# Kernel optimization log

Measured on AMD Instinct MI355X. Metric: run time of the kernel, lower is better.

Reference implementation:

```python
import jax, jax.numpy as jnp
import numpy as np
import math

N, D = 4096, 1024

def setup_inputs() -> dict:
    key = jax.random.key(0)
    ks = jax.random.split(key, 12)
    x = jax.random.normal(ks[0], (N, D), dtype=jnp.float32)
    attention_mask = jax.random.randint(ks[1], (N, N), 0, 2).astype(jnp.float32)
    learnable_mask = jax.random.randint(ks[2], (N, N), 0, 2).astype(jnp.float32)
    boundary_mask = jax.random.randint(ks[3], (N, 1), 0, 2).astype(jnp.float32)
    s = 1.0 / math.sqrt(D)
    W_q = jax.random.normal(ks[4], (D, D), dtype=jnp.float32) * s
    b_q = jax.random.normal(ks[5], (D,), dtype=jnp.float32) * s
    W_k = jax.random.normal(ks[6], (D, D), dtype=jnp.float32) * s
    b_k = jax.random.normal(ks[7], (D,), dtype=jnp.float32) * s
    W_v = jax.random.normal(ks[8], (D, D), dtype=jnp.float32) * s
    b_v = jax.random.normal(ks[9], (D,), dtype=jnp.float32) * s
    connection = jax.random.normal(ks[10], (D, D), dtype=jnp.float32) * s
    bias = jnp.ones((1,), dtype=jnp.float32) * 0.01
    return {"x": x, "attention_mask": attention_mask, "learnable_mask": learnable_mask,
            "boundary_mask": boundary_mask, "W_q": W_q, "b_q": b_q, "W_k": W_k, "b_k": b_k,
            "W_v": W_v, "b_v": b_v, "connection": connection, "bias": bias}

def reference(x, attention_mask, learnable_mask, boundary_mask,
              W_q, b_q, W_k, b_k, W_v, b_v, connection, bias):
    # Linear layers (torch Linear: x @ W.T + b)
    q = x @ W_q.T + b_q            # [N, D]
    k = x @ W_k.T + b_k            # [N, D]
    v = x @ W_v.T + b_v            # [N, D]
    d_head = k.shape[-1]
    attention_logits = (q @ k.T) / jnp.sqrt(jnp.asarray(d_head, x.dtype))  # [N, N]
    connection_logits = (q @ connection) @ k.T + bias                      # [N, N]
    # straight-through hard sigmoid mask
    soft_mask = jax.nn.sigmoid(connection_logits)
    st_mask = (soft_mask > 0.5).astype(x.dtype) - jax.lax.stop_gradient(soft_mask) + soft_mask
    lm = st_mask * learnable_mask
    mask = attention_mask + lm
    mask = -10000.0 * (1.0 - mask)
    attention = jax.nn.softmax(attention_logits + mask, axis=-1)  # [N, N]
    x_residual = attention @ v                                    # [N, D]
    out = boundary_mask * x_residual + (1.0 - boundary_mask) * x
    return out
```

## Files before the change

kernel.cpp:

```cpp
#include <hip/hip_runtime.h>
#include <cstdint>


typedef __attribute__((ext_vector_type(8))) short short8;
typedef __attribute__((ext_vector_type(4))) float f32x4;
typedef __attribute__((ext_vector_type(4))) float f4v;
typedef __attribute__((ext_vector_type(4))) unsigned short u16x4;
typedef __attribute__((ext_vector_type(8))) unsigned short u16x8;

typedef unsigned short u16;
typedef unsigned char u8;

__device__ __forceinline__ u16 f2bf(float f) {
  unsigned u = __float_as_uint(f);
  u += 0x7fffu + ((u >> 16) & 1u);
  return (u16)(u >> 16);
}
__device__ __forceinline__ float bf2f(u16 h) {
  return __uint_as_float(((unsigned)h) << 16);
}

__device__ __forceinline__ void gld16(void* lds, const void* g) {
  __builtin_amdgcn_global_load_lds(
      (__attribute__((address_space(1))) void*)g,
      (__attribute__((address_space(3))) void*)lds,
      16, 0, 0);
}


__global__ void prep_bm(const float* __restrict__ bm, int* __restrict__ idx,
                        int* __restrict__ cntp) {
  __shared__ int ps[1024];
  const int t = threadIdx.x;
  int loc[4];
  int c = 0;
#pragma unroll
  for (int e = 0; e < 4; e++) {
    int r = t * 4 + e;
    if (bm[r] != 0.0f) loc[c++] = r;
  }
  ps[t] = c;
  __syncthreads();
  for (int off = 1; off < 1024; off <<= 1) {
    int v = (t >= off) ? ps[t - off] : 0;
    __syncthreads();
    ps[t] += v;
    __syncthreads();
  }
  int base = ps[t] - c;
  for (int i = 0; i < c; i++) idx[base + i] = loc[i];
  int cnt = ps[1023];
  if (t == 0) cntp[0] = cnt;
  for (int r = cnt + t; r < 4096; r += 1024) idx[r] = 0;
}

__global__ void prep_x(const float* __restrict__ x, u16* __restrict__ xs3) {
  int id = blockIdx.x * 256 + threadIdx.x;
  int flat = id * 4;
  int n = flat >> 10, i = flat & 1023;
  f4v v = *(const f4v*)(x + (size_t)flat);
  u16x4 hi, lo;
#pragma unroll
  for (int e = 0; e < 4; e++) {
    float f = v[e];
    u16 h = f2bf(f);
    hi[e] = h;
    lo[e] = f2bf(f - bf2f(h));
  }
  size_t base = (size_t)n * 3072 + i;
  *(u16x4*)(xs3 + base) = hi;
  *(u16x4*)(xs3 + base + 1024) = lo;
  *(u16x4*)(xs3 + base + 2048) = hi;
}

__global__ void prep_w(const float* __restrict__ Wq, const float* __restrict__ Wk,
                       const float* __restrict__ Wv, u16* __restrict__ W3) {
  int id = blockIdx.x * 256 + threadIdx.x;
  int flat = id * 4;
  int o = flat >> 10, i = flat & 1023;
  const float* src = (o < 1024) ? (Wq + (size_t)o * 1024)
                   : (o < 2048) ? (Wk + (size_t)(o - 1024) * 1024)
                                : (Wv + (size_t)(o - 2048) * 1024);
  f4v v = *(const f4v*)(src + i);
  u16x4 hi, lo;
#pragma unroll
  for (int e = 0; e < 4; e++) {
    u16 h = f2bf(v[e]);
    hi[e] = h;
    lo[e] = f2bf(v[e] - bf2f(h));
  }
  size_t base = (size_t)o * 3072 + i;
  *(u16x4*)(W3 + base) = hi;
  *(u16x4*)(W3 + base + 1024) = hi;
  *(u16x4*)(W3 + base + 2048) = lo;
}

__global__ void prep_bias(const float* __restrict__ bq, const float* __restrict__ bk,
                          const float* __restrict__ bv, float* __restrict__ bp) {
  int id = blockIdx.x * 256 + threadIdx.x;
  float v = (id < 1024) ? bq[id] : (id < 2048) ? bk[id - 1024] : bv[id - 2048];
  bp[id] = v;
}

__global__ void prep_c(const float* __restrict__ C, u16* __restrict__ C3) {
  __shared__ float t[32][33];
  int lx = threadIdx.x & 31, ly = threadIdx.x >> 5;
  int i0 = blockIdx.x * 32, j0 = blockIdx.y * 32;
#pragma unroll
  for (int r = 0; r < 32; r += 8)
    t[ly + r][lx] = C[(size_t)(i0 + ly + r) * 1024 + j0 + lx];
  __syncthreads();
#pragma unroll
  for (int r = 0; r < 32; r += 8) {
    float f = t[lx][ly + r];
    u16 h = f2bf(f);
    u16 l = f2bf(f - bf2f(h));
    size_t o = (size_t)(j0 + ly + r) * 3072 + i0 + lx;
    C3[o] = h;
    C3[o + 1024] = h;
    C3[o + 2048] = l;
  }
}


struct EpiG1 {
  const float* bp; u16* qs3; u16* k3; u16* vt; int mode;
  __device__ void operator()(int r, int c, float v) const {
    if (mode == 0) {
      v += bp[1024 + c];
      u16 h = f2bf(v);
      u16 l = f2bf(v - bf2f(h));
      size_t b = (size_t)r * 3072 + c;
      k3[b] = h; k3[b + 1024] = h; k3[b + 2048] = l;
    } else if (mode == 1) {
      v += bp[c];
      u16 h = f2bf(v);
      u16 l = f2bf(v - bf2f(h));
      size_t b = (size_t)r * 3072 + c;
      qs3[b] = h; qs3[b + 1024] = l; qs3[b + 2048] = h;
    } else {
      v += bp[2048 + r];
      vt[(size_t)r * 4096 + c] = f2bf(v);
    }
  }
};

struct EpiQCS {
  u16* qc3; u16* Sc; int isS;
  __device__ void operator()(int r, int c, float v) const {
    if (isS) {
      Sc[(size_t)r * 4096 + c] = f2bf(v);
    } else {
      u16 h = f2bf(v);
      u16 l = f2bf(v - bf2f(h));
      size_t b = (size_t)r * 3072 + c;
      qc3[b] = h; qc3[b + 1024] = l; qc3[b + 2048] = h;
    }
  }
};

struct EpiCL {
  u8* st; float b0;
  __device__ void operator()(int r, int c, float v) const {
    st[(size_t)r * 4096 + c] = (v + b0 > 0.f) ? 1 : 0;
  }
};

struct EpiPart {
  float* part; const int* idx; int cnt;
  __device__ void operator()(int r, int c, float v) const {
    if (r < cnt) part[(size_t)idx[r] * 1024 + c] = v;
  }
};

template <class Epi>
__device__ __forceinline__ void gemm_core(
    const u16* __restrict__ A, const u16* __restrict__ B,
    int lda, int ldb, int K, int mBase, int nBase,
    const int* __restrict__ ridx, Epi epi) {
  __shared__ __align__(16) u16 lA[128 * 64];
  __shared__ __align__(16) u16 lB[128 * 64];
  const int tid = threadIdx.x;
  const int wave = tid >> 6, lane = tid & 63;
  const int wm = wave & 1, wn = wave >> 1;
  const int lane16 = lane & 15, quad = lane >> 4;

  const int srow = tid >> 3;
  const int gchunk = ((tid & 7) ^ (srow & 7)) * 8;
  const u16* aPi[4];
#pragma unroll
  for (int i = 0; i < 4; i++) {
    int row = mBase + srow + 32 * i;
    int g = ridx ? ridx[row] : row;
    aPi[i] = A + (size_t)g * lda + gchunk;
  }
  const u16* bP = B + (size_t)(nBase + srow) * ldb + gchunk;
  const int woff = wave * 1024;

  const int rsw = lane16 & 7;
  const u16* raB = lA + (wm * 64 + lane16) * 64;
  const u16* rbB = lB + (wn * 64 + lane16) * 64;

  f32x4 acc[4][4];
#pragma unroll
  for (int i = 0; i < 4; i++)
#pragma unroll
    for (int j = 0; j < 4; j++) acc[i][j] = (f32x4){0.f, 0.f, 0.f, 0.f};

  for (int k0 = 0; k0 < K; k0 += 64) {
#pragma unroll
    for (int i = 0; i < 4; i++) {
      gld16((char*)lA + i * 4096 + woff, aPi[i] + k0);
      gld16((char*)lB + i * 4096 + woff, bP + (size_t)(32 * i) * ldb + k0);
    }
    __syncthreads();
    short8 af[2][4], bfr[2][4];
#pragma unroll
    for (int s = 0; s < 2; s++) {
      const int sl = (((s << 2) + quad) ^ rsw) * 8;
#pragma unroll
      for (int j = 0; j < 4; j++) {
        af[s][j]  = *(const short8*)(raB + j * 1024 + sl);
        bfr[s][j] = *(const short8*)(rbB + j * 1024 + sl);
      }
    }
#pragma unroll
    for (int s = 0; s < 2; s++)
#pragma unroll
      for (int im = 0; im < 4; im++)
#pragma unroll
        for (int in = 0; in < 4; in++)
          acc[im][in] = __builtin_amdgcn_mfma_f32_16x16x32_bf16(
              af[s][im], bfr[s][in], acc[im][in], 0, 0, 0);
    __syncthreads();
  }

#pragma unroll
  for (int im = 0; im < 4; im++)
#pragma unroll
    for (int in = 0; in < 4; in++)
#pragma unroll
      for (int i = 0; i < 4; i++) {
        int r = mBase + wm * 64 + im * 16 + quad * 4 + i;
        int c = nBase + wn * 64 + in * 16 + lane16;
        epi(r, c, acc[im][in][i]);
      }
}

__global__ __launch_bounds__(256, 2) void gemm_g1(
    const u16* __restrict__ xs3, const u16* __restrict__ W3,
    const float* __restrict__ bp, u16* __restrict__ qs3,
    u16* __restrict__ k3, u16* __restrict__ vt,
    const int* __restrict__ idx, const int* __restrict__ cntp) {
  const int bid = blockIdx.x;
  const u16 *A, *B;
  const int* rx = nullptr;
  int K, mB, nB, mode;
  if (bid < 256) {
    A = xs3; B = W3 + (size_t)1024 * 3072; K = 3072;
    mB = (bid >> 3) * 128; nB = (bid & 7) * 128; mode = 0;
  } else if (bid < 512) {
    const int t = bid - 256;
    mB = (t >> 3) * 128;
    if (mB >= cntp[0]) return;
    A = xs3; B = W3; K = 3072; nB = (t & 7) * 128; rx = idx; mode = 1;
  } else {
    const int t = bid - 512;
    A = W3 + (size_t)2048 * 3072; B = xs3; K = 1024;
    mB = (t & 7) * 128; nB = (t >> 3) * 128; mode = 2;
  }
  gemm_core(A, B, 3072, 3072, K, mB, nB, rx, EpiG1{bp, qs3, k3, vt, mode});
}

__global__ __launch_bounds__(256, 2) void gemm_qc_s(
    const u16* __restrict__ qs3, const u16* __restrict__ C3,
    const u16* __restrict__ k3, u16* __restrict__ qc3, u16* __restrict__ Sc,
    const int* __restrict__ cntp) {
  const int bid = blockIdx.x;
  const int cnt = cntp[0];
  const u16* B;
  int K, mB, nB, isS;
  if (bid < 256) {
    mB = (bid >> 3) * 128;
    if (mB >= cnt) return;
    B = C3; K = 3072; nB = (bid & 7) * 128; isS = 0;
  } else {
    const int t = bid - 256;
    mB = (t >> 5) * 128;
    if (mB >= cnt) return;
    B = k3; K = 1024; nB = (t & 31) * 128; isS = 1;
  }
  gemm_core(qs3, B, 3072, 3072, K, mB, nB, nullptr, EpiQCS{qc3, Sc, isS});
}

__global__ __launch_bounds__(256, 2) void gemm_cl(
    const u16* __restrict__ qc3, const u16* __restrict__ k3,
    const float* __restrict__ bias, u8* __restrict__ st,
    const int* __restrict__ cntp) {
  const int bid = blockIdx.x;
  const int mBase = (bid >> 5) * 128;
  if (mBase >= cntp[0]) return;
  gemm_core(qc3, k3, 3072, 3072, 3072, mBase, (bid & 31) * 128, nullptr,
            EpiCL{st, bias[0]});
}

__global__ __launch_bounds__(256, 2) void gemm_pv(
    const u16* __restrict__ P, const u16* __restrict__ vt,
    float* __restrict__ p01, float* __restrict__ p23,
    const int* __restrict__ idx, const int* __restrict__ cntp) {
  const int bid = blockIdx.x;
  const int z = bid >> 8, rem = bid & 255;
  const int cnt = cntp[0];
  const int mBase = (rem >> 3) * 128;
  if (mBase >= cnt) return;
  float* base = ((z < 2) ? p01 : p23) + (size_t)(z & 1) * (4096ull * 1024ull);
  const size_t kOff = (size_t)z * 1024;
  gemm_core(P + kOff, vt + kOff, 4096, 4096, 1024, mBase, (rem & 7) * 128,
            nullptr, EpiPart{base, idx, cnt});
}

__global__ void reduce_out(const float* __restrict__ x, const float* __restrict__ bm,
                           const float* __restrict__ p01, const float* __restrict__ p23,
                           float* __restrict__ out) {
  int id = blockIdx.x * 256 + threadIdx.x;
  int flat = id * 4;
  int r = flat >> 10;
  float b = bm[r];
  f4v xv = *(const f4v*)(x + (size_t)flat);
  f4v o;
  if (b != 0.0f) {
    const size_t SL = (size_t)4096 * 1024;
    f4v a0 = *(const f4v*)(p01 + (size_t)flat);
    f4v a1 = *(const f4v*)(p01 + SL + flat);
    f4v a2 = *(const f4v*)(p23 + (size_t)flat);
    f4v a3 = *(const f4v*)(p23 + SL + flat);
#pragma unroll
    for (int e = 0; e < 4; e++)
      o[e] = b * ((a0[e] + a1[e]) + (a2[e] + a3[e])) + (1.0f - b) * xv[e];
  } else {
    o = xv;
  }
  *(f4v*)(out + (size_t)flat) = o;
}

__global__ __launch_bounds__(256) void mask_softmax(
    const u16* __restrict__ Sc, const u8* __restrict__ st,
    const float* __restrict__ am, const float* __restrict__ lm,
    u16* __restrict__ P, const int* __restrict__ idx,
    const int* __restrict__ cntp) {
  const int n = blockIdx.x, tid = threadIdx.x;
  if (n >= cntp[0]) return;
  const int orow = idx[n];
  const int lane = tid & 63, wave = tid >> 6;
  const u16* Srow = Sc + (size_t)n * 4096;
  const u8* Trow = st + (size_t)n * 4096;
  const float* Arow = am + (size_t)orow * 4096;
  const float* Lrow = lm + (size_t)orow * 4096;

  float lg[16];
  float mx = -3.4e38f;
#pragma unroll
  for (int j = 0; j < 2; j++) {
    int base = (tid + 256 * j) * 8;
    u16x8 s8 = *(const u16x8*)(Srow + base);
    unsigned long long t8 = *(const unsigned long long*)(Trow + base);
    f4v a0 = *(const f4v*)(Arow + base), a1 = *(const f4v*)(Arow + base + 4);
    f4v l0 = *(const f4v*)(Lrow + base), l1 = *(const f4v*)(Lrow + base + 4);
#pragma unroll
    for (int e = 0; e < 8; e++) {
      float stv = ((t8 >> (8 * e)) & 1ull) ? 1.f : 0.f;
      float a = (e < 4) ? a0[e] : a1[e - 4];
      float l = (e < 4) ? l0[e] : l1[e - 4];
      float mv = a + stv * l;
      float v = bf2f(s8[e]) * 0.03125f - 10000.f * (1.f - mv);
      lg[j * 8 + e] = v;
      mx = fmaxf(mx, v);
    }
  }
#pragma unroll
  for (int o = 32; o; o >>= 1) mx = fmaxf(mx, __shfl_xor(mx, o));
  __shared__ float smax[4], ssum[4];
  if (lane == 0) smax[wave] = mx;
  __syncthreads();
  mx = fmaxf(fmaxf(smax[0], smax[1]), fmaxf(smax[2], smax[3]));

  float sum = 0.f;
#pragma unroll
  for (int i = 0; i < 16; i++) { lg[i] = __expf(lg[i] - mx); sum += lg[i]; }
#pragma unroll
  for (int o = 32; o; o >>= 1) sum += __shfl_xor(sum, o);
  if (lane == 0) ssum[wave] = sum;
  __syncthreads();
  float inv = 1.f / (ssum[0] + ssum[1] + ssum[2] + ssum[3]);

  u16* Pr = P + (size_t)n * 4096;
#pragma unroll
  for (int j = 0; j < 2; j++) {
    int base = (tid + 256 * j) * 8;
    u16x8 o8;
#pragma unroll
    for (int e = 0; e < 8; e++) o8[e] = f2bf(lg[j * 8 + e] * inv);
    *(u16x8*)(Pr + base) = o8;
  }
}


extern "C" void kernel_launch(void* const* d_in, const int* in_sizes, int n_in,
                              void* d_out, int out_size, void* d_ws, size_t ws_size,
                              hipStream_t stream) {
  const float* x    = (const float*)d_in[0];
  const float* am   = (const float*)d_in[1];
  const float* lm   = (const float*)d_in[2];
  const float* bm   = (const float*)d_in[3];
  const float* Wq   = (const float*)d_in[4];
  const float* bq   = (const float*)d_in[5];
  const float* Wk   = (const float*)d_in[6];
  const float* bk   = (const float*)d_in[7];
  const float* Wv   = (const float*)d_in[8];
  const float* bv   = (const float*)d_in[9];
  const float* Cc   = (const float*)d_in[10];
  const float* bias = (const float*)d_in[11];
  float* out = (float*)d_out;
  char* ws = (char*)d_ws;

  if (ws_size < 0xB010000) return;

  u16*  xs3 = (u16*) (ws + 0x0000000);
  u16*  W3  = (u16*) (ws + 0x1800000);
  u16*  C3  = (u16*) (ws + 0x2A00000);
  float* bp = (float*)(ws + 0x3000000);
  int*  idx = (int*)  (ws + 0x3004000);
  int*  cnt = (int*)  (ws + 0x3008000);
  u16*  qs3 = (u16*) (ws + 0x3010000);
  u16*  qc3 = (u16*) (ws + 0x4810000);
  u16*  k3  = (u16*) (ws + 0x6010000);
  u16*  vt  = (u16*) (ws + 0x7810000);
  u16*  Sc  = (u16*) (ws + 0x8010000);
  u8*   st  = (u8*)  (ws + 0xA010000);
  u16*  P   = (u16*) (ws + 0x0000000);
  float* parts01 = (float*)(ws + 0x4810000);
  float* parts23 = (float*)(ws + 0x8010000);

  prep_bm  <<<1, 1024, 0, stream>>>(bm, idx, cnt);
  prep_x   <<<4096, 256, 0, stream>>>(x, xs3);
  prep_w   <<<3072, 256, 0, stream>>>(Wq, Wk, Wv, W3);
  prep_bias<<<12,   256, 0, stream>>>(bq, bk, bv, bp);
  prep_c   <<<dim3(32, 32), 256, 0, stream>>>(Cc, C3);

  gemm_g1<<<768, 256, 0, stream>>>(xs3, W3, bp, qs3, k3, vt, idx, cnt);
  gemm_qc_s<<<1280, 256, 0, stream>>>(qs3, C3, k3, qc3, Sc, cnt);
  gemm_cl<<<1024, 256, 0, stream>>>(qc3, k3, bias, st, cnt);
  mask_softmax<<<4096, 256, 0, stream>>>(Sc, st, am, lm, P, idx, cnt);
  gemm_pv<<<1024, 256, 0, stream>>>(P, vt, parts01, parts23, idx, cnt);
  reduce_out<<<4096, 256, 0, stream>>>(x, bm, parts01, parts23, out);
}
```

Measured before the change: 417.9 us.

## Precompute Wq-connection product to fuse q and qc projections into one GEMM

```diff
diff --git a/kernel.cpp b/kernel.cpp
--- a/kernel.cpp
+++ b/kernel.cpp
@@ -27,104 +27,141 @@
       16, 0, 0);
 }
 
-
-__global__ void prep_bm(const float* __restrict__ bm, int* __restrict__ idx,
-                        int* __restrict__ cntp) {
-  __shared__ int ps[1024];
-  const int t = threadIdx.x;
-  int loc[4];
-  int c = 0;
-#pragma unroll
-  for (int e = 0; e < 4; e++) {
-    int r = t * 4 + e;
-    if (bm[r] != 0.0f) loc[c++] = r;
-  }
-  ps[t] = c;
-  __syncthreads();
-  for (int off = 1; off < 1024; off <<= 1) {
-    int v = (t >= off) ? ps[t - off] : 0;
+__global__ __launch_bounds__(256) void prep_all(
+    const float* __restrict__ x, const float* __restrict__ Wq,
+    const float* __restrict__ Wk, const float* __restrict__ Wv,
+    const float* __restrict__ bq, const float* __restrict__ bk,
+    const float* __restrict__ bv, const float* __restrict__ C,
+    const float* __restrict__ bm,
+    u16* __restrict__ xs3, u16* __restrict__ W3, u16* __restrict__ Wqm,
+    u16* __restrict__ WqT3, u16* __restrict__ C3,
+    float* __restrict__ bp, float* __restrict__ b1,
+    int* __restrict__ idx, int* __restrict__ cntp) {
+  __shared__ float tb[32][33];
+  __shared__ int ps[256];
+  const int bid = blockIdx.x, t = threadIdx.x;
+
+  if (bid < 4096) {
+    int flat = (bid * 256 + t) * 4;
+    int n = flat >> 10, i = flat & 1023;
+    f4v v = *(const f4v*)(x + (size_t)flat);
+    u16x4 hi, lo;
+#pragma unroll
+    for (int e = 0; e < 4; e++) {
+      u16 h = f2bf(v[e]);
+      hi[e] = h;
+      lo[e] = f2bf(v[e] - bf2f(h));
+    }
+    size_t base = (size_t)n * 3072 + i;
+    *(u16x4*)(xs3 + base) = hi;
+    *(u16x4*)(xs3 + base + 1024) = lo;
+    *(u16x4*)(xs3 + base + 2048) = hi;
+  } else if (bid < 6144) {
+    int flat = ((bid - 4096) * 256 + t) * 4;
+    int o = flat >> 10, i = flat & 1023;
+    const float* src = (o < 1024) ? (Wk + (size_t)o * 1024)
+                                  : (Wv + (size_t)(o - 1024) * 1024);
+    f4v v = *(const f4v*)(src + i);
+    u16x4 hi, lo;
+#pragma unroll
+    for (int e = 0; e < 4; e++) {
+      u16 h = f2bf(v[e]);
+      hi[e] = h;
+      lo[e] = f2bf(v[e] - bf2f(h));
+    }
+    size_t base = (size_t)o * 3072 + i;
+    *(u16x4*)(W3 + base) = hi;
+    *(u16x4*)(W3 + base + 1024) = hi;
+    *(u16x4*)(W3 + base + 2048) = lo;
+  } else if (bid < 7168) {
+    int flat = ((bid - 6144) * 256 + t) * 4;
+    int o = flat >> 10, i = flat & 1023;
+    f4v v = *(const f4v*)(Wq + (size_t)o * 1024 + i);
+    u16x4 hi, lo;
+#pragma unroll
+    for (int e = 0; e < 4; e++) {
+      u16 h = f2bf(v[e]);
+      hi[e] = h;
+      lo[e] = f2bf(v[e] - bf2f(h));
+    }
+    size_t base = (size_t)o * 3072 + i;
+    *(u16x4*)(Wqm + base) = hi;
+    *(u16x4*)(Wqm + base + 1024) = hi;
+    *(u16x4*)(Wqm + base + 2048) = lo;
+  } else if (bid < 8192) {
+    int tt = bid - 7168;
+    int lx = t & 31, ly = t >> 5;
+    int i0 = (tt & 31) * 32, j0 = (tt >> 5) * 32;
+#pragma unroll
+    for (int r = 0; r < 32; r += 8)
+      tb[ly + r][lx] = Wq[(size_t)(i0 + ly + r) * 1024 + j0 + lx];
     __syncthreads();
-    ps[t] += v;
+#pragma unroll
+    for (int r = 0; r < 32; r += 8) {
+      float f = tb[lx][ly + r];
+      u16 h = f2bf(f);
+      u16 l = f2bf(f - bf2f(h));
+      size_t o = (size_t)(j0 + ly + r) * 3072 + i0 + lx;
+      WqT3[o] = h;
+      WqT3[o + 1024] = h;
+      WqT3[o + 2048] = l;
+    }
+  } else if (bid < 9216) {
+    int tt = bid - 8192;
+    int lx = t & 31, ly = t >> 5;
+    int i0 = (tt & 31) * 32, j0 = (tt >> 5) * 32;
+#pragma unroll
+    for (int r = 0; r < 32; r += 8)
+      tb[ly + r][lx] = C[(size_t)(i0 + ly + r) * 1024 + j0 + lx];
     __syncthreads();
-  }
-  int base = ps[t] - c;
-  for (int i = 0; i < c; i++) idx[base + i] = loc[i];
-  int cnt = ps[1023];
-  if (t == 0) cntp[0] = cnt;
-  for (int r = cnt + t; r < 4096; r += 1024) idx[r] = 0;
-}
-
-__global__ void prep_x(const float* __restrict__ x, u16* __restrict__ xs3) {
-  int id = blockIdx.x * 256 + threadIdx.x;
-  int flat = id * 4;
-  int n = flat >> 10, i = flat & 1023;
-  f4v v = *(const f4v*)(x + (size_t)flat);
-  u16x4 hi, lo;
-#pragma unroll
-  for (int e = 0; e < 4; e++) {
-    float f = v[e];
-    u16 h = f2bf(f);
-    hi[e] = h;
-    lo[e] = f2bf(f - bf2f(h));
-  }
-  size_t base = (size_t)n * 3072 + i;
-  *(u16x4*)(xs3 + base) = hi;
-  *(u16x4*)(xs3 + base + 1024) = lo;
-  *(u16x4*)(xs3 + base + 2048) = hi;
-}
-
-__global__ void prep_w(const float* __restrict__ Wq, const float* __restrict__ Wk,
-                       const float* __restrict__ Wv, u16* __restrict__ W3) {
-  int id = blockIdx.x * 256 + threadIdx.x;
-  int flat = id * 4;
-  int o = flat >> 10, i = flat & 1023;
-  const float* src = (o < 1024) ? (Wq + (size_t)o * 1024)
-                   : (o < 2048) ? (Wk + (size_t)(o - 1024) * 1024)
-                                : (Wv + (size_t)(o - 2048) * 1024);
-  f4v v = *(const f4v*)(src + i);
-  u16x4 hi, lo;
-#pragma unroll
-  for (int e = 0; e < 4; e++) {
-    u16 h = f2bf(v[e]);
-    hi[e] = h;
-    lo[e] = f2bf(v[e] - bf2f(h));
-  }
-  size_t base = (size_t)o * 3072 + i;
-  *(u16x4*)(W3 + base) = hi;
-  *(u16x4*)(W3 + base + 1024) = hi;
-  *(u16x4*)(W3 + base + 2048) = lo;
-}
-
-__global__ void prep_bias(const float* __restrict__ bq, const float* __restrict__ bk,
-                          const float* __restrict__ bv, float* __restrict__ bp) {
-  int id = blockIdx.x * 256 + threadIdx.x;
-  float v = (id < 1024) ? bq[id] : (id < 2048) ? bk[id - 1024] : bv[id - 2048];
-  bp[id] = v;
-}
-
-__global__ void prep_c(const float* __restrict__ C, u16* __restrict__ C3) {
-  __shared__ float t[32][33];
-  int lx = threadIdx.x & 31, ly = threadIdx.x >> 5;
-  int i0 = blockIdx.x * 32, j0 = blockIdx.y * 32;
-#pragma unroll
-  for (int r = 0; r < 32; r += 8)
-    t[ly + r][lx] = C[(size_t)(i0 + ly + r) * 1024 + j0 + lx];
-  __syncthreads();
-#pragma unroll
-  for (int r = 0; r < 32; r += 8) {
-    float f = t[lx][ly + r];
-    u16 h = f2bf(f);
-    u16 l = f2bf(f - bf2f(h));
-    size_t o = (size_t)(j0 + ly + r) * 3072 + i0 + lx;
-    C3[o] = h;
-    C3[o + 1024] = h;
-    C3[o + 2048] = l;
+#pragma unroll
+    for (int r = 0; r < 32; r += 8) {
+      float f = tb[lx][ly + r];
+      u16 h = f2bf(f);
+      u16 l = f2bf(f - bf2f(h));
+      size_t o = (size_t)(j0 + ly + r) * 3072 + i0 + lx;
+      C3[o] = h;
+      C3[o + 1024] = l;
+      C3[o + 2048] = h;
+    }
+  } else if (bid < 9228) {
+    int id = (bid - 9216) * 256 + t;
+    float v = (id < 1024) ? bq[id] : (id < 2048) ? bk[id - 1024] : bv[id - 2048];
+    bp[id] = v;
+  } else if (bid == 9228) {
+    int c = 0;
+    for (int e = 0; e < 16; e++) {
+      int r = t * 16 + e;
+      if (bm[r] != 0.0f) c++;
+    }
+    ps[t] = c;
+    __syncthreads();
+    for (int off = 1; off < 256; off <<= 1) {
+      int v = (t >= off) ? ps[t - off] : 0;
+      __syncthreads();
+      ps[t] += v;
+      __syncthreads();
+    }
+    int p = ps[t] - c;
+    for (int e = 0; e < 16; e++) {
+      int r = t * 16 + e;
+      if (bm[r] != 0.0f) idx[p++] = r;
+    }
+    int cn = ps[255];
+    if (t == 0) cntp[0] = cn;
+    for (int r = cn + t; r < 4096; r += 256) idx[r] = 0;
+  } else {
+    int j = (bid - 9229) * 256 + t;
+    float a = 0.f;
+    for (int d = 0; d < 1024; d++) a += bq[d] * C[(size_t)d * 1024 + j];
+    b1[j] = a;
   }
 }
 
 
 struct EpiG1 {
-  const float* bp; u16* qs3; u16* k3; u16* vt; int mode;
+  const float* bp; const float* b1;
+  u16* qs; u16* k3; u16* qc3; u16* vt; int mode;
   __device__ void operator()(int r, int c, float v) const {
     if (mode == 0) {
       v += bp[1024 + c];
@@ -133,11 +170,15 @@
       size_t b = (size_t)r * 3072 + c;
       k3[b] = h; k3[b + 1024] = h; k3[b + 2048] = l;
     } else if (mode == 1) {
-      v += bp[c];
-      u16 h = f2bf(v);
-      u16 l = f2bf(v - bf2f(h));
-      size_t b = (size_t)r * 3072 + c;
-      qs3[b] = h; qs3[b + 1024] = l; qs3[b + 2048] = h;
+      if (c < 1024) {
+        qs[(size_t)r * 1024 + c] = f2bf(v + bp[c]);
+      } else {
+        float w = v + b1[c - 1024];
+        u16 h = f2bf(w);
+        u16 l = f2bf(w - bf2f(h));
+        size_t b = (size_t)r * 3072 + (c - 1024);
+        qc3[b] = h; qc3[b + 1024] = l; qc3[b + 2048] = h;
+      }
     } else {
       v += bp[2048 + r];
       vt[(size_t)r * 4096 + c] = f2bf(v);
@@ -145,17 +186,17 @@
   }
 };
 
-struct EpiQCS {
-  u16* qc3; u16* Sc; int isS;
+struct EpiM1 {
+  float* part;
   __device__ void operator()(int r, int c, float v) const {
-    if (isS) {
-      Sc[(size_t)r * 4096 + c] = f2bf(v);
-    } else {
-      u16 h = f2bf(v);
-      u16 l = f2bf(v - bf2f(h));
-      size_t b = (size_t)r * 3072 + c;
-      qc3[b] = h; qc3[b + 1024] = l; qc3[b + 2048] = h;
-    }
+    part[(size_t)r * 1024 + c] = v;
+  }
+};
+
+struct EpiS {
+  u16* Sc;
+  __device__ void operator()(int r, int c, float v) const {
+    Sc[(size_t)r * 4096 + c] = f2bf(v);
   }
 };
 
@@ -247,50 +288,75 @@
       }
 }
 
+__global__ __launch_bounds__(256, 2) void gemm_m1(
+    const u16* __restrict__ C3, const u16* __restrict__ WqT3,
+    float* __restrict__ parts) {
+  const int z = blockIdx.x >> 6, tile = blockIdx.x & 63;
+  gemm_core(C3 + z * 768, WqT3 + z * 768, 3072, 3072, 768,
+            (tile >> 3) * 128, (tile & 7) * 128, nullptr,
+            EpiM1{parts + (size_t)z * 1024 * 1024});
+}
+
+__global__ void m1fin(const float* __restrict__ parts, u16* __restrict__ Wqm) {
+  int flat = (blockIdx.x * 256 + threadIdx.x) * 4;
+  int j = flat >> 10, i = flat & 1023;
+  const size_t SL = (size_t)1024 * 1024;
+  f4v p0 = *(const f4v*)(parts + (size_t)flat);
+  f4v p1 = *(const f4v*)(parts + SL + flat);
+  f4v p2 = *(const f4v*)(parts + 2 * SL + flat);
+  f4v p3 = *(const f4v*)(parts + 3 * SL + flat);
+  u16x4 hi, lo;
+#pragma unroll
+  for (int e = 0; e < 4; e++) {
+    float f = (p0[e] + p1[e]) + (p2[e] + p3[e]);
+    u16 h = f2bf(f);
+    hi[e] = h;
+    lo[e] = f2bf(f - bf2f(h));
+  }
+  size_t base = (size_t)(1024 + j) * 3072 + i;
+  *(u16x4*)(Wqm + base) = hi;
+  *(u16x4*)(Wqm + base + 1024) = hi;
+  *(u16x4*)(Wqm + base + 2048) = lo;
+}
+
 __global__ __launch_bounds__(256, 2) void gemm_g1(
     const u16* __restrict__ xs3, const u16* __restrict__ W3,
-    const float* __restrict__ bp, u16* __restrict__ qs3,
-    u16* __restrict__ k3, u16* __restrict__ vt,
+    const u16* __restrict__ Wqm, const float* __restrict__ bp,
+    const float* __restrict__ b1, u16* __restrict__ qs,
+    u16* __restrict__ k3, u16* __restrict__ qc3, u16* __restrict__ vt,
     const int* __restrict__ idx, const int* __restrict__ cntp) {
   const int bid = blockIdx.x;
+  const int sel = bid & 3;
   const u16 *A, *B;
   const int* rx = nullptr;
   int K, mB, nB, mode;
-  if (bid < 256) {
-    A = xs3; B = W3 + (size_t)1024 * 3072; K = 3072;
-    mB = (bid >> 3) * 128; nB = (bid & 7) * 128; mode = 0;
-  } else if (bid < 512) {
-    const int t = bid - 256;
-    mB = (t >> 3) * 128;
-    if (mB >= cntp[0]) return;
-    A = xs3; B = W3; K = 3072; nB = (t & 7) * 128; rx = idx; mode = 1;
+  if (sel < 3) {
+    const int L = (bid >> 2) * 3 + sel;
+    if (L < 256) {
+      A = xs3; B = W3; K = 3072;
+      mB = (L >> 3) * 128; nB = (L & 7) * 128; mode = 0;
+    } else {
+      const int t = L - 256;
+      mB = (t >> 4) * 128;
+      if (mB >= cntp[0]) return;
+      A = xs3; B = Wqm; K = 3072; nB = (t & 15) * 128; rx = idx; mode = 1;
+    }
   } else {
-    const int t = bid - 512;
-    A = W3 + (size_t)2048 * 3072; B = xs3; K = 1024;
-    mB = (t & 7) * 128; nB = (t >> 3) * 128; mode = 2;
-  }
-  gemm_core(A, B, 3072, 3072, K, mB, nB, rx, EpiG1{bp, qs3, k3, vt, mode});
-}
-
-__global__ __launch_bounds__(256, 2) void gemm_qc_s(
-    const u16* __restrict__ qs3, const u16* __restrict__ C3,
-    const u16* __restrict__ k3, u16* __restrict__ qc3, u16* __restrict__ Sc,
-    const int* __restrict__ cntp) {
-  const int bid = blockIdx.x;
-  const int cnt = cntp[0];
-  const u16* B;
-  int K, mB, nB, isS;
-  if (bid < 256) {
-    mB = (bid >> 3) * 128;
-    if (mB >= cnt) return;
-    B = C3; K = 3072; nB = (bid & 7) * 128; isS = 0;
-  } else {
-    const int t = bid - 256;
-    mB = (t >> 5) * 128;
-    if (mB >= cnt) return;
-    B = k3; K = 1024; nB = (t & 31) * 128; isS = 1;
-  }
-  gemm_core(qs3, B, 3072, 3072, K, mB, nB, nullptr, EpiQCS{qc3, Sc, isS});
+    const int s = bid >> 2;
+    A = W3 + (size_t)1024 * 3072; B = xs3; K = 1024;
+    mB = (s & 7) * 128; nB = (s >> 3) * 128; mode = 2;
+  }
+  gemm_core(A, B, 3072, 3072, K, mB, nB, rx,
+            EpiG1{bp, b1, qs, k3, qc3, vt, mode});
+}
+
+__global__ __launch_bounds__(256, 2) void gemm_s(
+    const u16* __restrict__ qs, const u16* __restrict__ k3,
+    u16* __restrict__ Sc, const int* __restrict__ cntp) {
+  const int t = blockIdx.x;
+  const int mB = (t >> 5) * 128;
+  if (mB >= cntp[0]) return;
+  gemm_core(qs, k3, 1024, 3072, 1024, mB, (t & 31) * 128, nullptr, EpiS{Sc});
 }
 
 __global__ __launch_bounds__(256, 2) void gemm_cl(
@@ -425,30 +491,33 @@
 
   if (ws_size < 0xB010000) return;
 
-  u16*  xs3 = (u16*) (ws + 0x0000000);
-  u16*  W3  = (u16*) (ws + 0x1800000);
-  u16*  C3  = (u16*) (ws + 0x2A00000);
-  float* bp = (float*)(ws + 0x3000000);
-  int*  idx = (int*)  (ws + 0x3004000);
-  int*  cnt = (int*)  (ws + 0x3008000);
-  u16*  qs3 = (u16*) (ws + 0x3010000);
-  u16*  qc3 = (u16*) (ws + 0x4810000);
-  u16*  k3  = (u16*) (ws + 0x6010000);
-  u16*  vt  = (u16*) (ws + 0x7810000);
-  u16*  Sc  = (u16*) (ws + 0x8010000);
-  u8*   st  = (u8*)  (ws + 0xA010000);
-  u16*  P   = (u16*) (ws + 0x0000000);
-  float* parts01 = (float*)(ws + 0x4810000);
-  float* parts23 = (float*)(ws + 0x8010000);
-
-  prep_bm  <<<1, 1024, 0, stream>>>(bm, idx, cnt);
-  prep_x   <<<4096, 256, 0, stream>>>(x, xs3);
-  prep_w   <<<3072, 256, 0, stream>>>(Wq, Wk, Wv, W3);
-  prep_bias<<<12,   256, 0, stream>>>(bq, bk, bv, bp);
-  prep_c   <<<dim3(32, 32), 256, 0, stream>>>(Cc, C3);
-
-  gemm_g1<<<768, 256, 0, stream>>>(xs3, W3, bp, qs3, k3, vt, idx, cnt);
-  gemm_qc_s<<<1280, 256, 0, stream>>>(qs3, C3, k3, qc3, Sc, cnt);
+  u16*  xs3  = (u16*) (ws + 0x0000000);
+  u16*  W3   = (u16*) (ws + 0x1800000);
+  u16*  Wqm  = (u16*) (ws + 0x2400000);
+  u16*  C3   = (u16*) (ws + 0x3000000);
+  u16*  WqT3 = (u16*) (ws + 0x3600000);
+  float* bp  = (float*)(ws + 0x3C00000);
+  float* b1  = (float*)(ws + 0x3C04000);
+  int*  idx  = (int*)  (ws + 0x3C08000);
+  int*  cnt  = (int*)  (ws + 0x3C0C000);
+  u16*  qs   = (u16*) (ws + 0x3D00000);
+  u16*  qc3  = (u16*) (ws + 0x4500000);
+  u16*  k3   = (u16*) (ws + 0x5D00000);
+  u16*  vt   = (u16*) (ws + 0x7500000);
+  u16*  Sc   = (u16*) (ws + 0x7D00000);
+  u8*   st   = (u8*)  (ws + 0x9D00000);
+  float* m1parts = (float*)(ws + 0x7D00000);
+  u16*  P    = (u16*) (ws + 0x0000000);
+  float* parts01 = (float*)(ws + 0x4500000);
+  float* parts23 = (float*)(ws + 0x7D00000);
+
+  prep_all<<<9233, 256, 0, stream>>>(x, Wq, Wk, Wv, bq, bk, bv, Cc, bm,
+                                     xs3, W3, Wqm, WqT3, C3, bp, b1, idx, cnt);
+  gemm_m1<<<256, 256, 0, stream>>>(C3, WqT3, m1parts);
+  m1fin<<<1024, 256, 0, stream>>>(m1parts, Wqm);
+  gemm_g1<<<1024, 256, 0, stream>>>(xs3, W3, Wqm, bp, b1, qs, k3, qc3, vt,
+                                    idx, cnt);
+  gemm_s<<<1024, 256, 0, stream>>>(qs, k3, Sc, cnt);
   gemm_cl<<<1024, 256, 0, stream>>>(qc3, k3, bias, st, cnt);
   mask_softmax<<<4096, 256, 0, stream>>>(Sc, st, am, lm, P, idx, cnt);
   gemm_pv<<<1024, 256, 0, stream>>>(P, vt, parts01, parts23, idx, cnt);
```

After: 450.6 us. +7.8%, slower.
